# Kernel optimization log

Hardware: AMD Instinct MI355X
Metric: run time of the kernel (lower is better)

Reference implementation:

```python
import jax, jax.numpy as jnp
import numpy as np
from jax import lax

EMBED_DIM = 1024
NUM_HEADS = 8
KEY_DIM = EMBED_DIM // NUM_HEADS  # 128
B, H, W = 2, 48, 48
N = H * W


def _rope(t, sin, cos):
    # t: [..., d]; sin/cos broadcastable to t
    x1 = t[..., ::2]
    x2 = t[..., 1::2]
    rot = jnp.stack([-x2, x1], axis=-1).reshape(t.shape)  # interleave (-x2, x1)
    return t * cos - rot * sin


def setup_inputs() -> dict:
    key = jax.random.key(0)
    ks = jax.random.split(key, 16)
    C = EMBED_DIM
    w = 0.02
    return {
        "x": jax.random.normal(ks[0], (B, H, W, C), jnp.float32),
        "sin": jax.random.normal(ks[1], (H, W, KEY_DIM), jnp.float32),
        "cos": jax.random.normal(ks[2], (H, W, KEY_DIM), jnp.float32),
        "mask": jax.random.normal(ks[3], (NUM_HEADS, N, N), jnp.float32),
        "Wq": jax.random.normal(ks[4], (C, C), jnp.float32) * w,
        "bq": jax.random.normal(ks[5], (C,), jnp.float32) * w,
        "Wk": jax.random.normal(ks[6], (C, C), jnp.float32) * w,
        "bk": jax.random.normal(ks[7], (C,), jnp.float32) * w,
        "Wv": jax.random.normal(ks[8], (C, C), jnp.float32) * w,
        "bv": jax.random.normal(ks[9], (C,), jnp.float32) * w,
        "lepe_w": jax.random.normal(ks[10], (5, 5, 1, C), jnp.float32) * w,  # HWIO, groups=C
        "lepe_b": jax.random.normal(ks[11], (C,), jnp.float32) * w,
        "Wo": jax.random.normal(ks[12], (C, C), jnp.float32) * w,
        "bo": jnp.zeros((C,), jnp.float32),
    }


def reference(x, sin, cos, mask, Wq, bq, Wk, bk, Wv, bv, lepe_w, lepe_b, Wo, bo):
    Bb, Hh, Ww, C = x.shape
    nh, kd = NUM_HEADS, KEY_DIM
    scaling = kd ** -0.5

    q = x @ Wq.T + bq                     # [B,H,W,C]
    k = (x @ Wk.T + bk) * scaling         # [B,H,W,C]
    v = x @ Wv.T + bv                     # [B,H,W,C]

    # depthwise 5x5 lepe on NHWC
    lepe = lax.conv_general_dilated(
        v, lepe_w, window_strides=(1, 1), padding="SAME",
        dimension_numbers=("NHWC", "HWIO", "NHWC"),
        feature_group_count=C,
    ) + lepe_b

    # [B,H,W,C] -> [B,nh,H,W,kd]
    qh = q.reshape(Bb, Hh, Ww, nh, kd).transpose(0, 3, 1, 2, 4)
    kh = k.reshape(Bb, Hh, Ww, nh, kd).transpose(0, 3, 1, 2, 4)

    sin_ = sin[None, None]  # [1,1,H,W,kd]
    cos_ = cos[None, None]
    qh = _rope(qh, sin_, cos_)
    kh = _rope(kh, sin_, cos_)

    qf = qh.reshape(Bb, nh, Hh * Ww, kd)  # [B,nh,N,kd]
    kf = kh.reshape(Bb, nh, Hh * Ww, kd)
    vf = v.reshape(Bb, Hh, Ww, nh, kd).transpose(0, 3, 1, 2, 4).reshape(Bb, nh, Hh * Ww, kd)

    attn = jnp.einsum("bhnd,bhmd->bhnm", qf, kf) + mask  # [B,nh,N,N]
    attn = jax.nn.softmax(attn, axis=-1)
    out = jnp.einsum("bhnm,bhmd->bhnd", attn, vf)         # [B,nh,N,kd]

    out = out.transpose(0, 2, 1, 3).reshape(Bb, Hh, Ww, nh * kd)
    out = out + lepe
    return out @ Wo.T + bo
```

## Files before the change

kernel.cpp:

```cpp
#include <hip/hip_runtime.h>
#include <hip/hip_bf16.h>
#include <stdint.h>

typedef __bf16 bf16_t;
typedef __bf16 bf16x8 __attribute__((ext_vector_type(8)));
typedef __bf16 bf16x4 __attribute__((ext_vector_type(4)));
typedef float f32x4 __attribute__((ext_vector_type(4)));
typedef unsigned int u32x4 __attribute__((ext_vector_type(4)));

#define MFMA16(A, B, C) __builtin_amdgcn_mfma_f32_16x16x32_bf16(A, B, C, 0, 0, 0)

__device__ inline void dma16(const void* g, void* l) {
    __builtin_amdgcn_global_load_lds(
        (const __attribute__((address_space(1))) unsigned int*)g,
        (__attribute__((address_space(3))) unsigned int*)l, 16, 0, 0);
}

__device__ inline unsigned pack2(float a, float b) {
    unsigned short ua = __builtin_bit_cast(unsigned short, (bf16_t)a);
    unsigned short ub = __builtin_bit_cast(unsigned short, (bf16_t)b);
    return (unsigned)ua | ((unsigned)ub << 16);
}

__global__ __launch_bounds__(256)
void cvt_kernel(const float* __restrict__ in, bf16_t* __restrict__ outp, int n8)
{
    int i = blockIdx.x * 256 + threadIdx.x;
    if (i >= n8) return;
    const float* p = in + (size_t)i * 8;
    f32x4 a = *(const f32x4*)p;
    f32x4 b = *(const f32x4*)(p + 4);
    bf16x8 r;
    r[0] = (bf16_t)a[0]; r[1] = (bf16_t)a[1]; r[2] = (bf16_t)a[2]; r[3] = (bf16_t)a[3];
    r[4] = (bf16_t)b[0]; r[5] = (bf16_t)b[1]; r[6] = (bf16_t)b[2]; r[7] = (bf16_t)b[3];
    *(bf16x8*)(outp + (size_t)i * 8) = r;
}

__global__ __launch_bounds__(256)
void gemm_bt_kernel(const bf16_t* __restrict__ A, const bf16_t* __restrict__ W,
                    const float* __restrict__ bias, void* __restrict__ outp,
                    int mode, float scale,
                    const float* __restrict__ sinp, const float* __restrict__ cosp)
{
    const int K = 1024;
    __shared__ __align__(16) char lds[16384];
    char* As = lds;
    char* Bs = lds + 8192;

    const int t = threadIdx.x;
    const int w = t >> 6, l = t & 63;
    const int wm = w >> 1, wn = w & 1;
    const int m0 = blockIdx.x * 128;
    const int n0 = blockIdx.y * 128;
    const int lr = l & 15;
    const int kch = (l >> 4) * 8;

    const f32x4 zz = {0.f, 0.f, 0.f, 0.f};
    f32x4 acc[4][4];
#pragma unroll
    for (int i = 0; i < 4; i++)
#pragma unroll
        for (int j = 0; j < 4; j++) acc[i][j] = zz;

    for (int k0 = 0; k0 < K; k0 += 32) {
        __syncthreads();
#pragma unroll
        for (int i = 0; i < 2; i++) {
            int f = w * 2 + i;
            dma16(A + (size_t)(m0 + f * 16 + lr) * K + k0 + kch, As + f * 1024);
            dma16(W + (size_t)(n0 + f * 16 + lr) * K + k0 + kch, Bs + f * 1024);
        }
        __syncthreads();
        bf16x8 af[4], bfg[4];
#pragma unroll
        for (int mt = 0; mt < 4; mt++)
            af[mt] = *(const bf16x8*)(As + ((wm * 4 + mt) * 64 + l) * 16);
#pragma unroll
        for (int nt = 0; nt < 4; nt++)
            bfg[nt] = *(const bf16x8*)(Bs + ((wn * 4 + nt) * 64 + l) * 16);
#pragma unroll
        for (int mt = 0; mt < 4; mt++)
#pragma unroll
            for (int nt = 0; nt < 4; nt++)
                acc[mt][nt] = MFMA16(af[mt], bfg[nt], acc[mt][nt]);
    }

    const int quad = l >> 4, lc = l & 15;
#pragma unroll
    for (int mt = 0; mt < 4; mt++) {
#pragma unroll
        for (int nt = 0; nt < 4; nt++) {
            int gn = n0 + wn * 64 + nt * 16 + lc;
            float bv = bias[gn];
            int gm0 = m0 + wm * 64 + mt * 16 + quad * 4;
            if (mode == 0) {
                float* o32 = (float*)outp;
#pragma unroll
                for (int r = 0; r < 4; r++)
                    o32[(size_t)(gm0 + r) * 1024 + gn] = acc[mt][nt][r] + bv;
            } else if (mode == 1) {
                bf16_t* ob = (bf16_t*)outp;
                int h = gn >> 7, d = gn & 127;
#pragma unroll
                for (int r = 0; r < 4; r++) {
                    int gm = gm0 + r;
                    int b = gm / 2304;
                    int pos = gm - b * 2304;
                    float val = acc[mt][nt][r] + bv;
                    float pv = __shfl_xor(val, 1);
                    float sn = sinp[pos * 128 + d];
                    float cs = cosp[pos * 128 + d];
                    float res = (d & 1) ? (val * cs - pv * sn) : (val * cs + pv * sn);
                    ob[(((size_t)b * 8 + h) * 2304 + pos) * 128 + d] = (bf16_t)(res * scale);
                }
            } else {
                bf16_t* ob = (bf16_t*)outp;
                int h = gn >> 7, d = gn & 127;
                int b = gm0 / 2304;
                int pos0 = gm0 - b * 2304;
                bf16x4 s4;
#pragma unroll
                for (int r = 0; r < 4; r++)
                    s4[r] = (bf16_t)(acc[mt][nt][r] + bv);
                *(bf16x4*)(ob + (((size_t)b * 8 + h) * 128 + d) * 2304 + pos0) = s4;
            }
        }
    }
}

__global__ __launch_bounds__(256)
void attn_kernel(const bf16_t* __restrict__ q, const bf16_t* __restrict__ k,
                 const bf16_t* __restrict__ vt, const float* __restrict__ mask,
                 bf16_t* __restrict__ o)
{
    const int N = 2304;
    __shared__ __align__(16) char lds[32768];
    char* Ks = lds;
    char* Vts = lds + 16384;

    const int t = threadIdx.x;
    const int w = t >> 6, l = t & 63;
    const int quad = l >> 4, lc = l & 15;

    const int bh = blockIdx.y;
    const int b = bh >> 3, h = bh & 7;
    const int q0 = blockIdx.x * 64;
    const int qrow = q0 + w * 16 + lc;

    const bf16_t* qb = q + (size_t)bh * N * 128;
    const bf16_t* kb = k + (size_t)bh * N * 128;
    const bf16_t* vtb = vt + (size_t)bh * 128 * N;
    const float* mq = mask + (size_t)h * N * N + (size_t)qrow * N + quad * 4;

    bf16x8 qf[4];
#pragma unroll
    for (int kc = 0; kc < 4; kc++)
        qf[kc] = *(const bf16x8*)(qb + (size_t)qrow * 128 + kc * 32 + quad * 8);

    const f32x4 zz = {0.f, 0.f, 0.f, 0.f};
    float Mr = -1e30f, Lr = 0.f;
    f32x4 Oacc[8];
#pragma unroll
    for (int i = 0; i < 8; i++) Oacc[i] = zz;

    for (int kv0 = 0; kv0 < N; kv0 += 64) {
        __syncthreads();
#pragma unroll
        for (int i = 0; i < 4; i++) {
            int f = w * 4 + i;
            dma16(kb + (size_t)(kv0 + (f >> 2) * 16 + lc) * 128 + (f & 3) * 32 + quad * 8,
                  Ks + f * 1024);
            dma16(vtb + (size_t)((f >> 1) * 16 + lc) * N + kv0 + (f & 1) * 32 + quad * 8,
                  Vts + f * 1024);
        }
        __syncthreads();

        f32x4 s[4];
#pragma unroll
        for (int nt = 0; nt < 4; nt++) {
            f32x4 a = zz;
#pragma unroll
            for (int kc = 0; kc < 4; kc++) {
                bf16x8 kf = *(const bf16x8*)(Ks + ((nt * 4 + kc) * 64 + l) * 16);
                a = MFMA16(kf, qf[kc], a);
            }
            f32x4 mv = *(const f32x4*)(mq + kv0 + nt * 16);
            s[nt] = a + mv;
        }

        float mx = fmaxf(fmaxf(fmaxf(s[0][0], s[0][1]), fmaxf(s[0][2], s[0][3])),
                         fmaxf(fmaxf(s[1][0], s[1][1]), fmaxf(s[1][2], s[1][3])));
        mx = fmaxf(mx, fmaxf(fmaxf(fmaxf(s[2][0], s[2][1]), fmaxf(s[2][2], s[2][3])),
                             fmaxf(fmaxf(s[3][0], s[3][1]), fmaxf(s[3][2], s[3][3]))));
        mx = fmaxf(mx, __shfl_xor(mx, 16));
        mx = fmaxf(mx, __shfl_xor(mx, 32));
        float mnew = fmaxf(Mr, mx);
        float alpha = __expf(Mr - mnew);
        Mr = mnew;

        float rs = 0.f;
        unsigned pw[4][2];
#pragma unroll
        for (int nt = 0; nt < 4; nt++) {
            float p0 = __expf(s[nt][0] - mnew);
            float p1 = __expf(s[nt][1] - mnew);
            float p2 = __expf(s[nt][2] - mnew);
            float p3 = __expf(s[nt][3] - mnew);
            rs += (p0 + p1) + (p2 + p3);
            pw[nt][0] = pack2(p0, p1);
            pw[nt][1] = pack2(p2, p3);
        }
        rs += __shfl_xor(rs, 16);
        rs += __shfl_xor(rs, 32);
        Lr = Lr * alpha + rs;

#pragma unroll
        for (int dt = 0; dt < 8; dt++)
#pragma unroll
            for (int r = 0; r < 4; r++)
                Oacc[dt][r] *= alpha;

#pragma unroll
        for (int pc = 0; pc < 2; pc++) {
            u32x4 wv;
#pragma unroll
            for (int jp = 0; jp < 4; jp++) {
                int src = ((quad & 1) * 2 + (jp >> 1)) * 16 + lc;
                int t0 = __shfl((int)pw[pc * 2 + 0][jp & 1], src);
                int t1 = __shfl((int)pw[pc * 2 + 1][jp & 1], src);
                wv[jp] = (quad >> 1) ? (unsigned)t1 : (unsigned)t0;
            }
            bf16x8 pf = __builtin_bit_cast(bf16x8, wv);
#pragma unroll
            for (int dt = 0; dt < 8; dt++) {
                bf16x8 vf = *(const bf16x8*)(Vts + ((dt * 2 + pc) * 64 + l) * 16);
                Oacc[dt] = MFMA16(vf, pf, Oacc[dt]);
            }
        }
    }

    float inv = 1.f / Lr;
#pragma unroll
    for (int dt = 0; dt < 8; dt++) {
        bf16x4 s4;
#pragma unroll
        for (int r = 0; r < 4; r++) s4[r] = (bf16_t)(Oacc[dt][r] * inv);
        *(bf16x4*)(o + ((size_t)b * N + qrow) * 1024 + h * 128 + dt * 16 + quad * 4) = s4;
    }
}

__global__ __launch_bounds__(256)
void lepe_kernel(const bf16_t* __restrict__ vt, const float* __restrict__ wgt,
                 const float* __restrict__ lb, const bf16_t* __restrict__ o,
                 bf16_t* __restrict__ ab)
{
    __shared__ __align__(16) bf16_t sv[5 * 48 * 128];
    const int bh = blockIdx.y;
    const int b = bh >> 3, h = bh & 7;
    const int y0 = blockIdx.x;
    const int t = threadIdx.x;

#pragma unroll
    for (int it = 0; it < 15; it++) {
        int idx = t + it * 256;
        int ck = idx % 6;
        int dy = idx / 6;
        int d = dy & 127, yloc = dy >> 7;
        int y = y0 - 2 + yloc;
        bf16x8 vvv;
#pragma unroll
        for (int j = 0; j < 8; j++) vvv[j] = (bf16_t)0.f;
        if (y >= 0 && y < 48)
            vvv = *(const bf16x8*)(vt + ((size_t)bh * 128 + d) * 2304 + y * 48 + ck * 8);
        int x0 = ck * 8;
#pragma unroll
        for (int j = 0; j < 8; j++)
            sv[(yloc * 48 + x0 + j) * 128 + d] = vvv[j];
    }
    __syncthreads();

    const int d0 = (t & 15) * 8;
    const int xb = t >> 4;
    float acc[3][8];
    f32x4 b0 = *(const f32x4*)(lb + h * 128 + d0);
    f32x4 b1 = *(const f32x4*)(lb + h * 128 + d0 + 4);
#pragma unroll
    for (int c = 0; c < 3; c++)
#pragma unroll
        for (int j = 0; j < 4; j++) { acc[c][j] = b0[j]; acc[c][4 + j] = b1[j]; }

#pragma unroll
    for (int ky = 0; ky < 5; ky++) {
#pragma unroll
        for (int kx = 0; kx < 5; kx++) {
            const float* wp = wgt + (size_t)(ky * 5 + kx) * 1024 + h * 128 + d0;
            f32x4 w0 = *(const f32x4*)wp;
            f32x4 w1 = *(const f32x4*)(wp + 4);
#pragma unroll
            for (int c = 0; c < 3; c++) {
                int xx = xb + c * 16 + kx - 2;
                if (xx < 0 || xx >= 48) continue;
                bf16x8 vv = *(const bf16x8*)(&sv[(ky * 48 + xx) * 128 + d0]);
#pragma unroll
                for (int j = 0; j < 4; j++) {
                    acc[c][j]     += (float)vv[j]     * w0[j];
                    acc[c][4 + j] += (float)vv[4 + j] * w1[j];
                }
            }
        }
    }
#pragma unroll
    for (int c = 0; c < 3; c++) {
        int x = xb + c * 16;
        size_t off = ((size_t)b * 2304 + y0 * 48 + x) * 1024 + h * 128 + d0;
        bf16x8 ov = *(const bf16x8*)(o + off);
        bf16x8 res;
#pragma unroll
        for (int j = 0; j < 8; j++) res[j] = (bf16_t)(acc[c][j] + (float)ov[j]);
        *(bf16x8*)(ab + off) = res;
    }
}

extern "C" void kernel_launch(void* const* d_in, const int* in_sizes, int n_in,
                              void* d_out, int out_size, void* d_ws, size_t ws_size,
                              hipStream_t stream)
{
    const float* x    = (const float*)d_in[0];
    const float* sin_ = (const float*)d_in[1];
    const float* cos_ = (const float*)d_in[2];
    const float* mask = (const float*)d_in[3];
    const float* Wq   = (const float*)d_in[4];
    const float* bq   = (const float*)d_in[5];
    const float* Wk   = (const float*)d_in[6];
    const float* bk   = (const float*)d_in[7];
    const float* Wv   = (const float*)d_in[8];
    const float* bv   = (const float*)d_in[9];
    const float* lw   = (const float*)d_in[10];
    const float* lb   = (const float*)d_in[11];
    const float* Wo   = (const float*)d_in[12];
    const float* bo   = (const float*)d_in[13];

    const size_t NB = (size_t)2 * 2304 * 1024;

    bf16_t* dout_b = (bf16_t*)d_out;
    bf16_t* x16 = dout_b;
    bf16_t* vtb = dout_b + NB;
    bf16_t* ob  = dout_b;

    bf16_t* qb   = (bf16_t*)d_ws;
    bf16_t* kb   = qb + NB;
    bf16_t* wbuf = kb + NB;
    bf16_t* ab   = qb;

    dim3 blk(256);
    const float kscale = 0.08838834764831845f;

    cvt_kernel<<<2304, blk, 0, stream>>>(x, x16, 589824);
    cvt_kernel<<<512, blk, 0, stream>>>(Wq, wbuf, 131072);
    gemm_bt_kernel<<<dim3(36, 8), blk, 0, stream>>>(x16, wbuf, bq, qb, 1, 1.0f, sin_, cos_);
    cvt_kernel<<<512, blk, 0, stream>>>(Wk, wbuf, 131072);
    gemm_bt_kernel<<<dim3(36, 8), blk, 0, stream>>>(x16, wbuf, bk, kb, 1, kscale, sin_, cos_);
    cvt_kernel<<<512, blk, 0, stream>>>(Wv, wbuf, 131072);
    gemm_bt_kernel<<<dim3(36, 8), blk, 0, stream>>>(x16, wbuf, bv, vtb, 2, 1.0f, nullptr, nullptr);
    cvt_kernel<<<512, blk, 0, stream>>>(Wo, wbuf, 131072);
    attn_kernel<<<dim3(36, 16), blk, 0, stream>>>(qb, kb, vtb, mask, ob);
    lepe_kernel<<<dim3(48, 16), blk, 0, stream>>>(vtb, lw, lb, ob, ab);
    gemm_bt_kernel<<<dim3(36, 8), blk, 0, stream>>>(ab, wbuf, bo, d_out, 0, 1.0f, nullptr, nullptr);
}
```

Before: 603.1 us.

## Double-buffer GEMM and attention LDS tiles and fuse QKV launches

Adds double-buffered LDS staging to the GEMM and attention kernels, so the next K/V (or A/W) tile and the next mask slice are prefetched while the current tile is computed, and each loop iteration needs one barrier instead of two. Merges the four weight conversions into one kernel and the three Q/K/V projections into a single launch with a grid of 864 blocks, which removes launch gaps and gives the GPU more parallel blocks. The cost is twice the LDS per block (64KB for attention, 32KB for the GEMMs), which may lower occupancy, and a larger wbuf that now holds all four weight matrices.

```diff
diff --git a/kernel.cpp b/kernel.cpp
--- a/kernel.cpp
+++ b/kernel.cpp
@@ -37,21 +37,34 @@
 }
 
 __global__ __launch_bounds__(256)
-void gemm_bt_kernel(const bf16_t* __restrict__ A, const bf16_t* __restrict__ W,
-                    const float* __restrict__ bias, void* __restrict__ outp,
-                    int mode, float scale,
-                    const float* __restrict__ sinp, const float* __restrict__ cosp)
+void cvt4_kernel(const float* __restrict__ W0, const float* __restrict__ W1,
+                 const float* __restrict__ W2, const float* __restrict__ W3,
+                 bf16_t* __restrict__ outp)
+{
+    int i = blockIdx.x * 256 + threadIdx.x;
+    int sel = i >> 17;
+    int j = i & 131071;
+    const float* src = sel == 0 ? W0 : sel == 1 ? W1 : sel == 2 ? W2 : W3;
+    const float* p = src + (size_t)j * 8;
+    f32x4 a = *(const f32x4*)p;
+    f32x4 b = *(const f32x4*)(p + 4);
+    bf16x8 r;
+    r[0] = (bf16_t)a[0]; r[1] = (bf16_t)a[1]; r[2] = (bf16_t)a[2]; r[3] = (bf16_t)a[3];
+    r[4] = (bf16_t)b[0]; r[5] = (bf16_t)b[1]; r[6] = (bf16_t)b[2]; r[7] = (bf16_t)b[3];
+    *(bf16x8*)(outp + (size_t)i * 8) = r;
+}
+
+__device__ __forceinline__
+void gemm_core(const bf16_t* __restrict__ A, const bf16_t* __restrict__ W,
+               const float* __restrict__ bias, void* __restrict__ outp,
+               int mode, float scale,
+               const float* __restrict__ sinp, const float* __restrict__ cosp,
+               int m0, int n0, char* lds)
 {
     const int K = 1024;
-    __shared__ __align__(16) char lds[16384];
-    char* As = lds;
-    char* Bs = lds + 8192;
-
     const int t = threadIdx.x;
     const int w = t >> 6, l = t & 63;
     const int wm = w >> 1, wn = w & 1;
-    const int m0 = blockIdx.x * 128;
-    const int n0 = blockIdx.y * 128;
     const int lr = l & 15;
     const int kch = (l >> 4) * 8;
 
@@ -62,27 +75,40 @@
 #pragma unroll
         for (int j = 0; j < 4; j++) acc[i][j] = zz;
 
+#pragma unroll
+    for (int i = 0; i < 2; i++) {
+        int f = w * 2 + i;
+        dma16(A + (size_t)(m0 + f * 16 + lr) * K + kch, lds + f * 1024);
+        dma16(W + (size_t)(n0 + f * 16 + lr) * K + kch, lds + 8192 + f * 1024);
+    }
+    __syncthreads();
+
+    int bo = 0;
     for (int k0 = 0; k0 < K; k0 += 32) {
-        __syncthreads();
-#pragma unroll
-        for (int i = 0; i < 2; i++) {
-            int f = w * 2 + i;
-            dma16(A + (size_t)(m0 + f * 16 + lr) * K + k0 + kch, As + f * 1024);
-            dma16(W + (size_t)(n0 + f * 16 + lr) * K + k0 + kch, Bs + f * 1024);
-        }
-        __syncthreads();
+        int kn = k0 + 32;
+        if (kn < K) {
+            int nb = bo ^ 16384;
+#pragma unroll
+            for (int i = 0; i < 2; i++) {
+                int f = w * 2 + i;
+                dma16(A + (size_t)(m0 + f * 16 + lr) * K + kn + kch, lds + nb + f * 1024);
+                dma16(W + (size_t)(n0 + f * 16 + lr) * K + kn + kch, lds + nb + 8192 + f * 1024);
+            }
+        }
         bf16x8 af[4], bfg[4];
 #pragma unroll
         for (int mt = 0; mt < 4; mt++)
-            af[mt] = *(const bf16x8*)(As + ((wm * 4 + mt) * 64 + l) * 16);
+            af[mt] = *(const bf16x8*)(lds + bo + ((wm * 4 + mt) * 64 + l) * 16);
 #pragma unroll
         for (int nt = 0; nt < 4; nt++)
-            bfg[nt] = *(const bf16x8*)(Bs + ((wn * 4 + nt) * 64 + l) * 16);
+            bfg[nt] = *(const bf16x8*)(lds + bo + 8192 + ((wn * 4 + nt) * 64 + l) * 16);
 #pragma unroll
         for (int mt = 0; mt < 4; mt++)
 #pragma unroll
             for (int nt = 0; nt < 4; nt++)
                 acc[mt][nt] = MFMA16(af[mt], bfg[nt], acc[mt][nt]);
+        __syncthreads();
+        bo ^= 16384;
     }
 
     const int quad = l >> 4, lc = l & 15;
@@ -129,14 +155,43 @@
 }
 
 __global__ __launch_bounds__(256)
+void gemm_bt_kernel(const bf16_t* __restrict__ A, const bf16_t* __restrict__ W,
+                    const float* __restrict__ bias, void* __restrict__ outp,
+                    int mode, float scale,
+                    const float* __restrict__ sinp, const float* __restrict__ cosp)
+{
+    __shared__ __align__(16) char lds[32768];
+    gemm_core(A, W, bias, outp, mode, scale, sinp, cosp,
+              blockIdx.x * 128, blockIdx.y * 128, lds);
+}
+
+__global__ __launch_bounds__(256)
+void gemm_qkv_kernel(const bf16_t* __restrict__ A, const bf16_t* __restrict__ Wall,
+                     const float* __restrict__ bq, const float* __restrict__ bk,
+                     const float* __restrict__ bv,
+                     void* __restrict__ qb, void* __restrict__ kb, void* __restrict__ vtb,
+                     const float* __restrict__ sinp, const float* __restrict__ cosp,
+                     float kscale)
+{
+    __shared__ __align__(16) char lds[32768];
+    int ny = blockIdx.y;
+    int third = ny >> 3;
+    int n0 = (ny & 7) * 128;
+    const bf16_t* W = Wall + (size_t)third * 1048576;
+    const float* bias = third == 0 ? bq : third == 1 ? bk : bv;
+    void* outp = third == 0 ? qb : third == 1 ? kb : vtb;
+    int mode = third == 2 ? 2 : 1;
+    float scale = third == 1 ? kscale : 1.0f;
+    gemm_core(A, W, bias, outp, mode, scale, sinp, cosp, blockIdx.x * 128, n0, lds);
+}
+
+__global__ __launch_bounds__(256)
 void attn_kernel(const bf16_t* __restrict__ q, const bf16_t* __restrict__ k,
                  const bf16_t* __restrict__ vt, const float* __restrict__ mask,
                  bf16_t* __restrict__ o)
 {
     const int N = 2304;
-    __shared__ __align__(16) char lds[32768];
-    char* Ks = lds;
-    char* Vts = lds + 16384;
+    __shared__ __align__(16) char lds[65536];
 
     const int t = threadIdx.x;
     const int w = t >> 6, l = t & 63;
@@ -157,23 +212,47 @@
     for (int kc = 0; kc < 4; kc++)
         qf[kc] = *(const bf16x8*)(qb + (size_t)qrow * 128 + kc * 32 + quad * 8);
 
+#pragma unroll
+    for (int i = 0; i < 4; i++) {
+        int f = w * 4 + i;
+        dma16(kb + (size_t)((f >> 2) * 16 + lc) * 128 + (f & 3) * 32 + quad * 8,
+              lds + f * 1024);
+        dma16(vtb + (size_t)((f >> 1) * 16 + lc) * N + (f & 1) * 32 + quad * 8,
+              lds + 16384 + f * 1024);
+    }
+    f32x4 mv[4];
+#pragma unroll
+    for (int nt = 0; nt < 4; nt++)
+        mv[nt] = *(const f32x4*)(mq + nt * 16);
+    __syncthreads();
+
     const f32x4 zz = {0.f, 0.f, 0.f, 0.f};
     float Mr = -1e30f, Lr = 0.f;
     f32x4 Oacc[8];
 #pragma unroll
     for (int i = 0; i < 8; i++) Oacc[i] = zz;
 
+    int bo = 0;
     for (int kv0 = 0; kv0 < N; kv0 += 64) {
-        __syncthreads();
-#pragma unroll
-        for (int i = 0; i < 4; i++) {
-            int f = w * 4 + i;
-            dma16(kb + (size_t)(kv0 + (f >> 2) * 16 + lc) * 128 + (f & 3) * 32 + quad * 8,
-                  Ks + f * 1024);
-            dma16(vtb + (size_t)((f >> 1) * 16 + lc) * N + kv0 + (f & 1) * 32 + quad * 8,
-                  Vts + f * 1024);
-        }
-        __syncthreads();
+        int nxt = kv0 + 64;
+        f32x4 mvn[4];
+        if (nxt < N) {
+            int nb = bo ^ 32768;
+#pragma unroll
+            for (int i = 0; i < 4; i++) {
+                int f = w * 4 + i;
+                dma16(kb + (size_t)(nxt + (f >> 2) * 16 + lc) * 128 + (f & 3) * 32 + quad * 8,
+                      lds + nb + f * 1024);
+                dma16(vtb + (size_t)((f >> 1) * 16 + lc) * N + nxt + (f & 1) * 32 + quad * 8,
+                      lds + nb + 16384 + f * 1024);
+            }
+#pragma unroll
+            for (int nt = 0; nt < 4; nt++)
+                mvn[nt] = *(const f32x4*)(mq + nxt + nt * 16);
+        }
+
+        const char* Ks = lds + bo;
+        const char* Vts = lds + bo + 16384;
 
         f32x4 s[4];
 #pragma unroll
@@ -184,8 +263,7 @@
                 bf16x8 kf = *(const bf16x8*)(Ks + ((nt * 4 + kc) * 64 + l) * 16);
                 a = MFMA16(kf, qf[kc], a);
             }
-            f32x4 mv = *(const f32x4*)(mq + kv0 + nt * 16);
-            s[nt] = a + mv;
+            s[nt] = a + mv[nt];
         }
 
         float mx = fmaxf(fmaxf(fmaxf(s[0][0], s[0][1]), fmaxf(s[0][2], s[0][3])),
@@ -236,6 +314,13 @@
                 bf16x8 vf = *(const bf16x8*)(Vts + ((dt * 2 + pc) * 64 + l) * 16);
                 Oacc[dt] = MFMA16(vf, pf, Oacc[dt]);
             }
+        }
+
+        __syncthreads();
+        if (nxt < N) {
+#pragma unroll
+            for (int nt = 0; nt < 4; nt++) mv[nt] = mvn[nt];
+            bo ^= 32768;
         }
     }
 
@@ -356,14 +441,11 @@
     const float kscale = 0.08838834764831845f;
 
     cvt_kernel<<<2304, blk, 0, stream>>>(x, x16, 589824);
-    cvt_kernel<<<512, blk, 0, stream>>>(Wq, wbuf, 131072);
-    gemm_bt_kernel<<<dim3(36, 8), blk, 0, stream>>>(x16, wbuf, bq, qb, 1, 1.0f, sin_, cos_);
-    cvt_kernel<<<512, blk, 0, stream>>>(Wk, wbuf, 131072);
-    gemm_bt_kernel<<<dim3(36, 8), blk, 0, stream>>>(x16, wbuf, bk, kb, 1, kscale, sin_, cos_);
-    cvt_kernel<<<512, blk, 0, stream>>>(Wv, wbuf, 131072);
-    gemm_bt_kernel<<<dim3(36, 8), blk, 0, stream>>>(x16, wbuf, bv, vtb, 2, 1.0f, nullptr, nullptr);
-    cvt_kernel<<<512, blk, 0, stream>>>(Wo, wbuf, 131072);
+    cvt4_kernel<<<2048, blk, 0, stream>>>(Wq, Wk, Wv, Wo, wbuf);
+    gemm_qkv_kernel<<<dim3(36, 24), blk, 0, stream>>>(x16, wbuf, bq, bk, bv,
+                                                      qb, kb, vtb, sin_, cos_, kscale);
     attn_kernel<<<dim3(36, 16), blk, 0, stream>>>(qb, kb, vtb, mask, ob);
     lepe_kernel<<<dim3(48, 16), blk, 0, stream>>>(vtb, lw, lb, ob, ab);
-    gemm_bt_kernel<<<dim3(36, 8), blk, 0, stream>>>(ab, wbuf, bo, d_out, 0, 1.0f, nullptr, nullptr);
-}
+    gemm_bt_kernel<<<dim3(36, 8), blk, 0, stream>>>(ab, wbuf + 3 * 1048576, bo,
+                                                    d_out, 0, 1.0f, nullptr, nullptr);
+}
```

Result: faster. 565.9 us (-6.2%).
